# Kernel tuning notes

Hardware: AMD Instinct MI355X
Metric: run time of the kernel (lower is better)

The kernel has to match this reference:

```python
import jax, jax.numpy as jnp
import numpy as np

EPS = 1e-8
LN_EPS = 1e-5
PSCALE = 10.0
P = 8  # n_points


def _bb_frames(Xn, Xca, Xc):
    # Gram-Schmidt rigid frame from N, CA, C (AlphaFold rigids_from_3_points).
    v1 = Xc - Xca
    v2 = Xn - Xca
    e1 = v1 / jnp.sqrt(jnp.sum(v1 * v1, -1, keepdims=True) + EPS)
    u2 = v2 - e1 * jnp.sum(e1 * v2, -1, keepdims=True)
    e2 = u2 / jnp.sqrt(jnp.sum(u2 * u2, -1, keepdims=True) + EPS)
    e3 = jnp.cross(e1, e2)
    R = jnp.stack([e1, e2, e3], axis=-1)  # [B,N,3,3], columns are basis vectors
    t = Xca / PSCALE                      # scale_translation(1/position_scale)
    return R, t


def _layernorm(x, g, b):
    mu = jnp.mean(x, -1, keepdims=True)
    var = jnp.mean((x - mu) ** 2, -1, keepdims=True)
    return (x - mu) / jnp.sqrt(var + LN_EPS) * g + b


def setup_inputs() -> dict:
    key = jax.random.key(0)
    ks = jax.random.split(key, 24)
    B, N, K, D, H = 8, 512, 32, 128, 128
    msg_in = 2 * D + D + 9 * P  # 456
    s = 0.02
    inp = {
        "h_V": jax.random.normal(ks[0], (B, N, D), jnp.float32),
        "h_E": jax.random.normal(ks[1], (B, N, K, D), jnp.float32),
        "X": jax.random.normal(ks[2], (B, N, 3, 3), jnp.float32),
        "mask_V": jnp.ones((B, N), jnp.float32),
        "mask_attend": jnp.ones((B, N, K), jnp.float32),
        "Wp": jax.random.normal(ks[3], (D, P * 3), jnp.float32) * s,
        "bp": jnp.zeros((P * 3,), jnp.float32),
        "Wm1": jax.random.normal(ks[4], (msg_in, H), jnp.float32) * s,
        "bm1": jnp.zeros((H,), jnp.float32),
        "Wm2": jax.random.normal(ks[5], (H, H), jnp.float32) * s,
        "bm2": jnp.zeros((H,), jnp.float32),
        "Wm3": jax.random.normal(ks[6], (H, H), jnp.float32) * s,
        "bm3": jnp.zeros((H,), jnp.float32),
        "g1": jnp.ones((H,), jnp.float32),
        "be1": jnp.zeros((H,), jnp.float32),
        "Wd1": jax.random.normal(ks[7], (H, 4 * H), jnp.float32) * s,
        "bd1": jnp.zeros((4 * H,), jnp.float32),
        "Wd2": jax.random.normal(ks[8], (4 * H, H), jnp.float32) * s,
        "bd2": jnp.zeros((H,), jnp.float32),
        "g2": jnp.ones((H,), jnp.float32),
        "be2": jnp.zeros((H,), jnp.float32),
        "E_idx": jax.random.randint(ks[9], (B, N, K), 0, N, jnp.int32),
    }
    return inp


def reference(h_V, h_E, X, mask_V, mask_attend,
              Wp, bp, Wm1, bm1, Wm2, bm2, Wm3, bm3, g1, be1,
              Wd1, bd1, Wd2, bd2, g2, be2, E_idx):
    B, N, K = E_idx.shape
    R, t = _bb_frames(X[..., 0, :], X[..., 1, :], X[..., 2, :])
    # local points [B,N,P,3]
    p_local = (h_V @ Wp + bp).reshape(B, N, P, 3)
    # global points: R @ p + t
    p_global = jnp.einsum('bnij,bnpj->bnpi', R, p_local) + t[:, :, None, :]
    bidx = jnp.arange(B)[:, None, None]
    nbr_pg = p_global[bidx, E_idx]  # [B,N,K,P,3]
    nbr_hV = h_V[bidx, E_idx]       # [B,N,K,D]
    # distances in global frame
    diff = p_global[:, :, None] - nbr_pg
    npg_norm = jnp.sqrt(jnp.sum(diff * diff, -1) + EPS)  # [B,N,K,P]
    # neighbor points in local frame: R^T (q - t)
    q = nbr_pg - t[:, :, None, None, :]
    nbr_pl = jnp.einsum('bnij,bnkpi->bnkpj', R, q)       # [B,N,K,P,3]
    npl_norm = jnp.sqrt(jnp.sum(nbr_pl * nbr_pl, -1) + EPS)
    pl_norm = jnp.sqrt(jnp.sum(p_local * p_local, -1) + EPS)  # [B,N,P]

    D = h_V.shape[-1]
    node_expand = jnp.broadcast_to(h_V[:, :, None, :], (B, N, K, D))
    pl_flat = jnp.broadcast_to(p_local[:, :, None], (B, N, K, P, 3)).reshape(B, N, K, P * 3)
    pl_norm_e = jnp.broadcast_to(pl_norm[:, :, None, :], (B, N, K, P))
    msg_in = jnp.concatenate([
        node_expand, h_E, nbr_hV,
        pl_flat, pl_norm_e,
        nbr_pl.reshape(B, N, K, P * 3), npl_norm, npg_norm,
    ], axis=-1)

    # node_message_fn: 3-layer MLP with relu
    m = jax.nn.relu(msg_in @ Wm1 + bm1)
    m = jax.nn.relu(m @ Wm2 + bm2)
    m = m @ Wm3 + bm3
    m = m * mask_attend[..., None]
    node_m = jnp.mean(m, axis=-2)  # [B,N,H]

    h = _layernorm(h_V + node_m, g1, be1)  # dropout = identity (eval)
    dense = jax.nn.relu(h @ Wd1 + bd1) @ Wd2 + bd2
    h = _layernorm(h + dense, g2, be2)
    h = h * mask_V[..., None]
    return h, h_E
```

## Files before the change

kernel.cpp:

```cpp
#include <hip/hip_runtime.h>
#include <hip/hip_bf16.h>

typedef __hip_bfloat16 bf16;
typedef __attribute__((ext_vector_type(8))) short s16x8;
typedef __attribute__((ext_vector_type(4))) float f32x4;

#define DEV __device__ __forceinline__

DEV float us2f(unsigned short u){ return __uint_as_float(((unsigned int)u) << 16); }
DEV unsigned short f2us(float f){
    __hip_bfloat16 h = __float2bfloat16(f);
    unsigned short r; __builtin_memcpy(&r, &h, 2); return r;
}
DEV unsigned pack2(float a, float b){ return (unsigned)f2us(a) | ((unsigned)f2us(b) << 16); }

template<bool F32> DEV float ldf(const void* p, long i){
    if (F32) return reinterpret_cast<const float*>(p)[i];
    return us2f(reinterpret_cast<const unsigned short*>(p)[i]);
}
template<bool F32> DEV unsigned short ld16(const void* p, long i){
    if (F32) return f2us(reinterpret_cast<const float*>(p)[i]);
    return reinterpret_cast<const unsigned short*>(p)[i];
}

union U16x8 { uint4 u; s16x8 v; };

DEV bool is_f32(const void* maskV){
    return reinterpret_cast<const unsigned short*>(maskV)[0] != 0x3F80;
}

struct __align__(16) PreSmem {
    union __align__(16) {
        unsigned short lwT[128*40];
        struct {
            unsigned short lwp[24*132];
            float sX[2][9], sR[2][9], st3[2][3], spl[2][24], hvs[2][128];
        } pr;
    } u;
};

template<bool F32>
DEV void pre_prep(const void* hV, const void* X, const void* Wp, const void* bp,
                  float* pg, float* pl, float* pln, float* Rw, float* tw,
                  PreSmem& s, int bid, int tid)
{
    auto& pr = s.u.pr;
    for (int e = tid; e < 3072; e += 128) {
        int i = e / 24, j = e - i*24;
        pr.lwp[j*132 + i] = ld16<F32>(Wp, e);
    }
    const int wv = tid >> 6, ln = tid & 63;
    const int n = bid*2 + wv;
    if (ln < 9) pr.sX[wv][ln] = ldf<F32>(X, (long)n*9 + ln);
    for (int i = ln; i < 128; i += 64) pr.hvs[wv][i] = ldf<F32>(hV, (long)n*128 + i);
    __syncthreads();

    if (ln == 0) {
        float Nx=pr.sX[wv][0],Ny=pr.sX[wv][1],Nz=pr.sX[wv][2];
        float Ax=pr.sX[wv][3],Ay=pr.sX[wv][4],Az=pr.sX[wv][5];
        float Cx=pr.sX[wv][6],Cy=pr.sX[wv][7],Cz=pr.sX[wv][8];
        float v1x=Cx-Ax, v1y=Cy-Ay, v1z=Cz-Az;
        float v2x=Nx-Ax, v2y=Ny-Ay, v2z=Nz-Az;
        float r1 = 1.f/sqrtf(v1x*v1x+v1y*v1y+v1z*v1z + 1e-8f);
        float e1x=v1x*r1, e1y=v1y*r1, e1z=v1z*r1;
        float dp = e1x*v2x+e1y*v2y+e1z*v2z;
        float u2x=v2x-e1x*dp, u2y=v2y-e1y*dp, u2z=v2z-e1z*dp;
        float r2 = 1.f/sqrtf(u2x*u2x+u2y*u2y+u2z*u2z + 1e-8f);
        float e2x=u2x*r2, e2y=u2y*r2, e2z=u2z*r2;
        float e3x = e1y*e2z - e1z*e2y;
        float e3y = e1z*e2x - e1x*e2z;
        float e3z = e1x*e2y - e1y*e2x;
        pr.sR[wv][0]=e1x; pr.sR[wv][1]=e2x; pr.sR[wv][2]=e3x;
        pr.sR[wv][3]=e1y; pr.sR[wv][4]=e2y; pr.sR[wv][5]=e3y;
        pr.sR[wv][6]=e1z; pr.sR[wv][7]=e2z; pr.sR[wv][8]=e3z;
        pr.st3[wv][0]=Ax*0.1f; pr.st3[wv][1]=Ay*0.1f; pr.st3[wv][2]=Az*0.1f;
    }
    if (ln < 24) {
        float acc = ldf<F32>(bp, ln);
        const unsigned short* wr = &pr.lwp[ln*132];
        #pragma unroll
        for (int c=0;c<16;c++){
            #pragma unroll
            for (int k=0;k<8;k++)
                acc += pr.hvs[wv][c*8+k] * us2f(wr[c*8+k]);
        }
        pr.spl[wv][ln] = acc;
    }
    __syncthreads();

    if (ln < 24) {
        pl[n*24+ln] = pr.spl[wv][ln];
        int p = ln/3, c = ln - p*3;
        float g = pr.sR[wv][c*3+0]*pr.spl[wv][p*3+0] + pr.sR[wv][c*3+1]*pr.spl[wv][p*3+1]
                + pr.sR[wv][c*3+2]*pr.spl[wv][p*3+2] + pr.st3[wv][c];
        pg[n*24+ln] = g;
    }
    if (ln < 9) Rw[n*9+ln] = pr.sR[wv][ln];
    if (ln < 3) tw[n*3+ln] = pr.st3[wv][ln];
    if (ln < 8) {
        float a=pr.spl[wv][ln*3], b=pr.spl[wv][ln*3+1], c=pr.spl[wv][ln*3+2];
        pln[n*8+ln] = sqrtf(a*a+b*b+c*c + 1e-8f);
    }
}

template<bool F32>
DEV void pre_uv(const void* hV, const void* bm1, const void* Wm1,
                unsigned short* Uw, unsigned short* Vw,
                PreSmem& s, int r0, int tid)
{
    const int lane = tid & 63, w2 = tid >> 6;
    const int lm = lane & 15, quad = lane >> 4;

    s16x8 af[4];
    #pragma unroll
    for (int kc=0; kc<4; ++kc) {
        long src = (long)(r0 + lm)*128 + kc*32 + quad*8;
        U16x8 pk;
        if (F32) {
            const float4* vp = reinterpret_cast<const float4*>(reinterpret_cast<const float*>(hV) + src);
            float4 x = vp[0], y = vp[1];
            pk.u.x = pack2(x.x,x.y); pk.u.y = pack2(x.z,x.w);
            pk.u.z = pack2(y.x,y.y); pk.u.w = pack2(y.z,y.w);
        } else {
            pk.u = *reinterpret_cast<const uint4*>(reinterpret_cast<const unsigned short*>(hV) + src);
        }
        af[kc] = pk.v;
    }

    f32x4 accU[4], accV[4];
    #pragma unroll
    for (int nt=0; nt<4; ++nt) {
        float b0 = ldf<F32>(bm1, 64*w2 + nt*16 + lm);
        f32x4 iv = {b0,b0,b0,b0};
        accU[nt] = iv;
        f32x4 zv = {0.f,0.f,0.f,0.f};
        accV[nt] = zv;
    }

    for (int p=0; p<8; ++p) {
        int k0 = (p<4) ? p*32 : 256 + (p-4)*32;
        __syncthreads();
        for (int e = tid; e < 4096; e += 128) {
            int kk = e >> 7, c = e & 127;
            s.u.lwT[c*40 + kk] = ld16<F32>(Wm1, (long)k0*128 + e);
        }
        __syncthreads();
        s16x8 a = af[p & 3];
        #pragma unroll
        for (int nt=0; nt<4; ++nt) {
            s16x8 bf = *reinterpret_cast<const s16x8*>(&s.u.lwT[(64*w2 + nt*16 + lm)*40 + quad*8]);
            if (p < 4) accU[nt] = __builtin_amdgcn_mfma_f32_16x16x32_bf16(a, bf, accU[nt], 0,0,0);
            else       accV[nt] = __builtin_amdgcn_mfma_f32_16x16x32_bf16(a, bf, accV[nt], 0,0,0);
        }
    }
    #pragma unroll
    for (int nt=0; nt<4; ++nt)
        #pragma unroll
        for (int r=0; r<4; ++r) {
            long o = (long)(r0 + quad*4 + r)*128 + 64*w2 + nt*16 + lm;
            Uw[o] = f2us(accU[nt][r]);
            Vw[o] = f2us(accV[nt][r]);
        }
}

template<bool F32>
DEV void pre_wt(const void* Wm1, const void* Wm2, const void* Wm3,
                const void* Wd1, const void* Wd2,
                unsigned short* wt1, unsigned short* wt2, unsigned short* wt3,
                unsigned short* wd1T, unsigned short* wd2T, long t)
{
    if (t < 61440) {
        int k = (int)(t >> 7), h = (int)(t & 127);
        wt1[(long)h*480 + k] = (k < 456) ? ld16<F32>(Wm1, (long)k*128 + h) : (unsigned short)0;
    } else if (t < 77824) {
        long t2 = t - 61440; int k = (int)(t2 >> 7), h = (int)(t2 & 127);
        wt2[(long)h*128 + k] = ld16<F32>(Wm2, (long)k*128 + h);
    } else if (t < 94208) {
        long t2 = t - 77824; int k = (int)(t2 >> 7), h = (int)(t2 & 127);
        wt3[(long)h*128 + k] = ld16<F32>(Wm3, (long)k*128 + h);
    } else if (t < 159744) {
        long t2 = t - 94208; int k = (int)(t2 >> 9), n = (int)(t2 & 511);
        wd1T[(long)n*128 + k] = ld16<F32>(Wd1, (long)k*512 + n);
    } else {
        long t2 = t - 159744; int k = (int)(t2 >> 7), n = (int)(t2 & 127);
        wd2T[(long)n*512 + k] = ld16<F32>(Wd2, (long)k*128 + n);
    }
}

__global__ __launch_bounds__(128) void pre_k(
    const void* __restrict__ hV, const void* __restrict__ X,
    const void* __restrict__ Wp, const void* __restrict__ bp,
    const void* __restrict__ Wm1, const void* __restrict__ bm1,
    const void* __restrict__ Wm2, const void* __restrict__ Wm3,
    const void* __restrict__ Wd1, const void* __restrict__ Wd2,
    float* __restrict__ pg, float* __restrict__ pl, float* __restrict__ pln,
    float* __restrict__ Rw, float* __restrict__ tw,
    unsigned short* __restrict__ Uw, unsigned short* __restrict__ Vw,
    unsigned short* __restrict__ wt1, unsigned short* __restrict__ wt2,
    unsigned short* __restrict__ wt3, unsigned short* __restrict__ wd1T,
    unsigned short* __restrict__ wd2T, const void* __restrict__ maskV)
{
    __shared__ PreSmem s;
    int bid = blockIdx.x, tid = threadIdx.x;
    bool f32 = is_f32(maskV);
    if (bid < 2048) {
        if (f32) pre_prep<true >(hV,X,Wp,bp,pg,pl,pln,Rw,tw,s,bid,tid);
        else     pre_prep<false>(hV,X,Wp,bp,pg,pl,pln,Rw,tw,s,bid,tid);
    } else if (bid < 2304) {
        int r0 = (bid - 2048) * 16;
        if (f32) pre_uv<true >(hV,bm1,Wm1,Uw,Vw,s,r0,tid);
        else     pre_uv<false>(hV,bm1,Wm1,Uw,Vw,s,r0,tid);
    } else {
        long t = (long)(bid - 2304)*128 + tid;
        if (f32) pre_wt<true >(Wm1,Wm2,Wm3,Wd1,Wd2,wt1,wt2,wt3,wd1T,wd2T,t);
        else     pre_wt<false>(Wm1,Wm2,Wm3,Wd1,Wd2,wt1,wt2,wt3,wd1T,wd2T,t);
    }
}

#define ASTRIDE 40
#define MSTRIDE 136

struct __align__(16) Mp1Smem {
    union __align__(16) {
        unsigned short geo[3][64*ASTRIDE];
        unsigned short m[64*MSTRIDE];
    } u;
    int   sj[64];
    float smka[64];
    float spg[2][24], spl[2][24], spln[2][8], sR[2][9], st3[2][3];
    unsigned short sU[2*128];
};

template<bool F32>
DEV void mpnn1_body(
    const void* hV, const void* hE, const void* maskA,
    const void* bm2, const void* bm3, const int* Eidx,
    const float* pg, const float* pl, const float* pln,
    const float* Rw, const float* tw,
    const unsigned short* wt1, const unsigned short* wt2, const unsigned short* wt3,
    const unsigned short* Uw, const unsigned short* Vw,
    float* nodemsg, void* outE, Mp1Smem& sm, int n0, int tid)
{
    const int lane = tid & 63, w = tid >> 6;
    const int lm = lane & 15, quad = lane >> 4;

    if (tid < 64) { int l = tid >> 5;
        sm.sj[tid] = (((n0+l) >> 9) << 9) + Eidx[(long)(n0+l)*32 + (tid & 31)];
    } else { int t = tid - 64; int l = t >> 5;
        sm.smka[t] = ldf<F32>(maskA, (long)(n0+l)*32 + (t & 31));
    }
    if (tid < 48)        { sm.spg[tid/24][tid%24] = pg[(n0+tid/24)*24 + tid%24]; }
    else if (tid < 96)   { int t=tid-48; sm.spl[t/24][t%24] = pl[(n0+t/24)*24 + t%24]; }
    else if (tid < 112)  { int t=tid-96; sm.spln[t>>3][t&7]  = pln[(n0+(t>>3))*8 + (t&7)]; }
    if (tid < 18)        { sm.sR[tid/9][tid%9] = Rw[(n0+tid/9)*9 + tid%9]; }
    else if (tid < 24)   { int t=tid-18; sm.st3[t/3][t%3] = tw[(n0+t/3)*3 + t%3]; }
    for (int e = tid; e < 256; e += 128)
        sm.sU[e] = Uw[(long)(n0 + (e>>7))*128 + (e & 127)];
    __syncthreads();

    #pragma unroll
    for (int pass=0; pass<4; ++pass) {
        int v = tid + pass*128;
        int row = v >> 3, p = v & 7, nd = row >> 5;
        int j = sm.sj[row];
        float qx = pg[j*24 + p*3 + 0];
        float qy = pg[j*24 + p*3 + 1];
        float qz = pg[j*24 + p*3 + 2];
        float dx = sm.spg[nd][p*3+0]-qx, dy = sm.spg[nd][p*3+1]-qy, dz = sm.spg[nd][p*3+2]-qz;
        float npg = sqrtf(dx*dx+dy*dy+dz*dz + 1e-8f);
        float ux = qx - sm.st3[nd][0], uy = qy - sm.st3[nd][1], uz = qz - sm.st3[nd][2];
        float l0 = sm.sR[nd][0]*ux + sm.sR[nd][3]*uy + sm.sR[nd][6]*uz;
        float l1 = sm.sR[nd][1]*ux + sm.sR[nd][4]*uy + sm.sR[nd][7]*uz;
        float l2v= sm.sR[nd][2]*ux + sm.sR[nd][5]*uy + sm.sR[nd][8]*uz;
        float npl = sqrtf(l0*l0+l1*l1+l2v*l2v + 1e-8f);
        unsigned short* C0 = sm.u.geo[0];
        unsigned short* C1 = sm.u.geo[1];
        unsigned short* C2 = sm.u.geo[2];
        C0[row*ASTRIDE + p*3+0] = f2us(sm.spl[nd][p*3+0]);
        C0[row*ASTRIDE + p*3+1] = f2us(sm.spl[nd][p*3+1]);
        C0[row*ASTRIDE + p*3+2] = f2us(sm.spl[nd][p*3+2]);
        C0[row*ASTRIDE + 24+p]  = f2us(sm.spln[nd][p]);
        C1[row*ASTRIDE + p*3+0] = f2us(l0);
        C1[row*ASTRIDE + p*3+1] = f2us(l1);
        C1[row*ASTRIDE + p*3+2] = f2us(l2v);
        C1[row*ASTRIDE + 24+p]  = f2us(npl);
        C2[row*ASTRIDE + p]     = f2us(npg);
    }
    for (int z = tid; z < 64*24; z += 128) {
        int row = z / 24, col = 8 + (z % 24);
        sm.u.geo[2][row*ASTRIDE + col] = 0;
    }
    __syncthreads();

    const unsigned short* wr1[4];
    #pragma unroll
    for (int nt=0; nt<4; ++nt) wr1[nt] = wt1 + (long)(64*w + nt*16 + lm)*480 + quad*8;

    f32x4 acc[4][4];
    {
        f32x4 zv = {0.f,0.f,0.f,0.f};
        #pragma unroll
        for (int mt=0; mt<4; ++mt)
            #pragma unroll
            for (int nt=0; nt<4; ++nt) acc[mt][nt] = zv;
    }

    #pragma unroll
    for (int c=0; c<4; ++c) {
        s16x8 av[4];
        #pragma unroll
        for (int mt=0; mt<4; ++mt) {
            int row16 = 16*mt + lm, nd = mt >> 1;
            long src = ((long)(n0+nd)*32 + (row16&31))*128 + c*32 + quad*8;
            U16x8 pk;
            if (F32) {
                const float4* vp = reinterpret_cast<const float4*>(reinterpret_cast<const float*>(hE) + src);
                float4 x = vp[0], y = vp[1];
                if (w == 0) {
                    float4* d = reinterpret_cast<float4*>(reinterpret_cast<float*>(outE) + src);
                    d[0] = x; d[1] = y;
                }
                pk.u.x = pack2(x.x,x.y); pk.u.y = pack2(x.z,x.w);
                pk.u.z = pack2(y.x,y.y); pk.u.w = pack2(y.z,y.w);
            } else {
                pk.u = *reinterpret_cast<const uint4*>(reinterpret_cast<const unsigned short*>(hE) + src);
                if (w == 0)
                    *reinterpret_cast<uint4*>(reinterpret_cast<unsigned short*>(outE) + src) = pk.u;
            }
            av[mt] = pk.v;
        }
        #pragma unroll
        for (int nt=0; nt<4; ++nt) {
            s16x8 bf = *reinterpret_cast<const s16x8*>(wr1[nt] + (long)(c+4)*32);
            #pragma unroll
            for (int mt=0; mt<4; ++mt)
                acc[mt][nt] = __builtin_amdgcn_mfma_f32_16x16x32_bf16(av[mt], bf, acc[mt][nt], 0,0,0);
        }
    }
    #pragma unroll
    for (int c=0; c<3; ++c) {
        s16x8 av[4];
        #pragma unroll
        for (int mt=0; mt<4; ++mt)
            av[mt] = *reinterpret_cast<const s16x8*>(&sm.u.geo[c][(16*mt+lm)*ASTRIDE + quad*8]);
        #pragma unroll
        for (int nt=0; nt<4; ++nt) {
            s16x8 bf = *reinterpret_cast<const s16x8*>(wr1[nt] + (long)(c+12)*32);
            #pragma unroll
            for (int mt=0; mt<4; ++mt)
                acc[mt][nt] = __builtin_amdgcn_mfma_f32_16x16x32_bf16(av[mt], bf, acc[mt][nt], 0,0,0);
        }
    }
    __syncthreads();

    #pragma unroll
    for (int mt=0; mt<4; ++mt)
        #pragma unroll
        for (int nt=0; nt<4; ++nt)
            #pragma unroll
            for (int r=0; r<4; ++r)
                sm.u.m[(16*mt + quad*4 + r)*MSTRIDE + 64*w + nt*16 + lm]
                    = f2us(acc[mt][nt][r]);

    const int row = tid >> 1, ch = tid & 1;
    const int jv = sm.sj[row];
    const unsigned short* vrow = Vw + (long)jv*128 + ch*64;
    uint4 pv[8];
    #pragma unroll
    for (int b=0;b<8;++b) pv[b] = *reinterpret_cast<const uint4*>(vrow + b*8);
    __syncthreads();

    {
        unsigned short* mrow = &sm.u.m[row*MSTRIDE + ch*64];
        const unsigned short* urow = &sm.sU[(row>>5)*128 + ch*64];
        #pragma unroll
        for (int b=0;b<8;++b) {
            U16x8 vm; vm.u = *reinterpret_cast<const uint4*>(mrow + b*8);
            U16x8 vv; vv.u = pv[b];
            float f[8];
            #pragma unroll
            for (int i=0;i<8;++i)
                f[i] = fmaxf(us2f((unsigned short)vm.v[i]) + us2f((unsigned short)vv.v[i])
                             + us2f(urow[b*8+i]), 0.f);
            uint4 o;
            o.x = pack2(f[0],f[1]); o.y = pack2(f[2],f[3]);
            o.z = pack2(f[4],f[5]); o.w = pack2(f[6],f[7]);
            *reinterpret_cast<uint4*>(mrow + b*8) = o;
        }
    }
    __syncthreads();

    #pragma unroll
    for (int nt=0; nt<4; ++nt) {
        float b0 = ldf<F32>(bm2, 64*w + nt*16 + lm);
        f32x4 iv = {b0,b0,b0,b0};
        #pragma unroll
        for (int mt=0; mt<4; ++mt) acc[mt][nt] = iv;
    }
    #pragma unroll
    for (int kc=0; kc<4; ++kc) {
        s16x8 av[4];
        #pragma unroll
        for (int mt=0; mt<4; ++mt)
            av[mt] = *reinterpret_cast<const s16x8*>(&sm.u.m[(16*mt+lm)*MSTRIDE + kc*32 + quad*8]);
        #pragma unroll
        for (int nt=0; nt<4; ++nt) {
            s16x8 bf = *reinterpret_cast<const s16x8*>(&wt2[(long)(64*w + nt*16 + lm)*128 + kc*32 + quad*8]);
            #pragma unroll
            for (int mt=0; mt<4; ++mt)
                acc[mt][nt] = __builtin_amdgcn_mfma_f32_16x16x32_bf16(av[mt], bf, acc[mt][nt], 0,0,0);
        }
    }
    __syncthreads();

    #pragma unroll
    for (int mt=0; mt<4; ++mt)
        #pragma unroll
        for (int nt=0; nt<4; ++nt)
            #pragma unroll
            for (int r=0; r<4; ++r)
                sm.u.m[(16*mt + quad*4 + r)*MSTRIDE + 64*w + nt*16 + lm]
                    = f2us(fmaxf(acc[mt][nt][r], 0.f));
    __syncthreads();

    #pragma unroll
    for (int nt=0; nt<4; ++nt) {
        float b0 = ldf<F32>(bm3, 64*w + nt*16 + lm);
        f32x4 iv = {b0,b0,b0,b0};
        #pragma unroll
        for (int mt=0; mt<4; ++mt) acc[mt][nt] = iv;
    }
    #pragma unroll
    for (int kc=0; kc<4; ++kc) {
        s16x8 av[4];
        #pragma unroll
        for (int mt=0; mt<4; ++mt)
            av[mt] = *reinterpret_cast<const s16x8*>(&sm.u.m[(16*mt+lm)*MSTRIDE + kc*32 + quad*8]);
        #pragma unroll
        for (int nt=0; nt<4; ++nt) {
            s16x8 bf = *reinterpret_cast<const s16x8*>(&wt3[(long)(64*w + nt*16 + lm)*128 + kc*32 + quad*8]);
            #pragma unroll
            for (int mt=0; mt<4; ++mt)
                acc[mt][nt] = __builtin_amdgcn_mfma_f32_16x16x32_bf16(av[mt], bf, acc[mt][nt], 0,0,0);
        }
    }

    #pragma unroll
    for (int nt=0; nt<4; ++nt) {
        float s0 = 0.f, s1 = 0.f;
        #pragma unroll
        for (int r=0; r<4; ++r) {
            s0 += acc[0][nt][r] * sm.smka[     quad*4 + r]
                + acc[1][nt][r] * sm.smka[16 + quad*4 + r];
            s1 += acc[2][nt][r] * sm.smka[32 + quad*4 + r]
                + acc[3][nt][r] * sm.smka[48 + quad*4 + r];
        }
        s0 += __shfl_xor(s0, 16); s0 += __shfl_xor(s0, 32);
        s1 += __shfl_xor(s1, 16); s1 += __shfl_xor(s1, 32);
        if (lane < 16) {
            nodemsg[(long)(n0  )*128 + 64*w + nt*16 + lane] = s0;
            nodemsg[(long)(n0+1)*128 + 64*w + nt*16 + lane] = s1;
        }
    }
}

__global__ __launch_bounds__(128) void mpnn1_k(
    const void* __restrict__ hV, const void* __restrict__ hE,
    const void* __restrict__ maskV, const void* __restrict__ maskA,
    const void* __restrict__ bm2, const void* __restrict__ bm3,
    const int* __restrict__ Eidx,
    const float* __restrict__ pg, const float* __restrict__ pl,
    const float* __restrict__ pln, const float* __restrict__ Rw,
    const float* __restrict__ tw,
    const unsigned short* __restrict__ wt1, const unsigned short* __restrict__ wt2,
    const unsigned short* __restrict__ wt3,
    const unsigned short* __restrict__ Uw, const unsigned short* __restrict__ Vw,
    float* __restrict__ nodemsg, void* __restrict__ dout)
{
    __shared__ Mp1Smem sm;
    int n0 = blockIdx.x * 2, tid = threadIdx.x;
    if (is_f32(maskV)) {
        void* outE = reinterpret_cast<float*>(dout) + 524288;
        mpnn1_body<true >(hV,hE,maskA,bm2,bm3,Eidx,pg,pl,pln,Rw,tw,wt1,wt2,wt3,Uw,Vw,nodemsg,outE,sm,n0,tid);
    } else {
        void* outE = reinterpret_cast<unsigned short*>(dout) + 524288;
        mpnn1_body<false>(hV,hE,maskA,bm2,bm3,Eidx,pg,pl,pln,Rw,tw,wt1,wt2,wt3,Uw,Vw,nodemsg,outE,sm,n0,tid);
    }
}

#define TSTRIDE 520

struct __align__(16) FfnSmem {
    unsigned short x1[16*MSTRIDE];
    union __align__(16) {
        unsigned short t1[16*TSTRIDE];
        float yf[16*132];
    } u;
};

template<bool F32>
DEV void ffn_body(const void* hV, const void* maskV, const float* nodemsg,
                  const void* g1, const void* be1, const void* bd1, const void* bd2,
                  const void* g2, const void* be2,
                  const unsigned short* wd1T, const unsigned short* wd2T,
                  void* out, FfnSmem& sm, int n0, int tid)
{
    const int lane = tid & 63, w = tid >> 6;
    const int lm = lane & 15, quad = lane >> 4;

    {
        const int r = tid >> 4, c0 = (tid & 15) * 8;
        const long nb = (long)(n0 + r)*128;
        float xv[8];
        float s1 = 0.f, s2 = 0.f;
        #pragma unroll
        for (int j=0; j<8; ++j) {
            float v = ldf<F32>(hV, nb + c0 + j) + nodemsg[nb + c0 + j] * (1.f/32.f);
            xv[j] = v; s1 += v; s2 += v*v;
        }
        s1 += __shfl_xor(s1,1); s1 += __shfl_xor(s1,2);
        s1 += __shfl_xor(s1,4); s1 += __shfl_xor(s1,8);
        s2 += __shfl_xor(s2,1); s2 += __shfl_xor(s2,2);
        s2 += __shfl_xor(s2,4); s2 += __shfl_xor(s2,8);
        float mu = s1 * (1.f/128.f);
        float var = s2 * (1.f/128.f) - mu*mu;
        float rs = 1.f/sqrtf(var + 1e-5f);
        #pragma unroll
        for (int j=0; j<8; ++j) {
            int c = c0 + j;
            sm.x1[r*MSTRIDE + c] = f2us((xv[j]-mu)*rs*ldf<F32>(g1, c) + ldf<F32>(be1, c));
        }
    }
    __syncthreads();

    {
        f32x4 t1a[8];
        #pragma unroll
        for (int nt=0; nt<8; ++nt) {
            float b0 = ldf<F32>(bd1, 128*w + nt*16 + lm);
            f32x4 iv = {b0,b0,b0,b0};
            t1a[nt] = iv;
        }
        #pragma unroll
        for (int kc=0; kc<4; ++kc) {
            s16x8 a = *reinterpret_cast<const s16x8*>(&sm.x1[lm*MSTRIDE + kc*32 + quad*8]);
            #pragma unroll
            for (int nt=0; nt<8; ++nt) {
                s16x8 bf = *reinterpret_cast<const s16x8*>(&wd1T[(long)(128*w + nt*16 + lm)*128 + kc*32 + quad*8]);
                t1a[nt] = __builtin_amdgcn_mfma_f32_16x16x32_bf16(a, bf, t1a[nt], 0,0,0);
            }
        }
        #pragma unroll
        for (int nt=0; nt<8; ++nt)
            #pragma unroll
            for (int r=0; r<4; ++r)
                sm.u.t1[(quad*4 + r)*TSTRIDE + 128*w + nt*16 + lm] = f2us(fmaxf(t1a[nt][r], 0.f));
    }
    __syncthreads();

    f32x4 yacc[2];
    #pragma unroll
    for (int nt=0; nt<2; ++nt) {
        float b0 = ldf<F32>(bd2, 32*w + nt*16 + lm);
        f32x4 iv = {b0,b0,b0,b0};
        yacc[nt] = iv;
    }
    #pragma unroll
    for (int kc=0; kc<16; ++kc) {
        s16x8 a = *reinterpret_cast<const s16x8*>(&sm.u.t1[lm*TSTRIDE + kc*32 + quad*8]);
        #pragma unroll
        for (int nt=0; nt<2; ++nt) {
            s16x8 bf = *reinterpret_cast<const s16x8*>(&wd2T[(long)(32*w + nt*16 + lm)*512 + kc*32 + quad*8]);
            yacc[nt] = __builtin_amdgcn_mfma_f32_16x16x32_bf16(a, bf, yacc[nt], 0,0,0);
        }
    }
    __syncthreads();

    #pragma unroll
    for (int nt=0; nt<2; ++nt)
        #pragma unroll
        for (int r=0; r<4; ++r) {
            int rr = quad*4 + r, c = 32*w + nt*16 + lm;
            sm.u.yf[rr*132 + c] = yacc[nt][r] + us2f(sm.x1[rr*MSTRIDE + c]);
        }
    __syncthreads();

    {
        const int r = tid >> 4, c0 = (tid & 15) * 8;
        float yv[8];
        float s1 = 0.f, s2 = 0.f;
        #pragma unroll
        for (int j=0; j<8; ++j) {
            float v = sm.u.yf[r*132 + c0 + j];
            yv[j] = v; s1 += v; s2 += v*v;
        }
        s1 += __shfl_xor(s1,1); s1 += __shfl_xor(s1,2);
        s1 += __shfl_xor(s1,4); s1 += __shfl_xor(s1,8);
        s2 += __shfl_xor(s2,1); s2 += __shfl_xor(s2,2);
        s2 += __shfl_xor(s2,4); s2 += __shfl_xor(s2,8);
        float mu = s1 * (1.f/128.f);
        float var = s2 * (1.f/128.f) - mu*mu;
        float rs = 1.f/sqrtf(var + 1e-5f);
        float mv = ldf<F32>(maskV, n0 + r);
        const long ob = (long)(n0 + r)*128 + c0;
        #pragma unroll
        for (int j=0; j<8; ++j) {
            int c = c0 + j;
            float v = ((yv[j]-mu)*rs*ldf<F32>(g2, c) + ldf<F32>(be2, c)) * mv;
            if (F32) reinterpret_cast<float*>(out)[ob + j] = v;
            else     reinterpret_cast<unsigned short*>(out)[ob + j] = f2us(v);
        }
    }
}

__global__ __launch_bounds__(256) void ffn_k(
    const void* __restrict__ hV, const void* __restrict__ maskV,
    const float* __restrict__ nodemsg,
    const void* __restrict__ g1, const void* __restrict__ be1,
    const void* __restrict__ bd1, const void* __restrict__ bd2,
    const void* __restrict__ g2, const void* __restrict__ be2,
    const unsigned short* __restrict__ wd1T, const unsigned short* __restrict__ wd2T,
    void* __restrict__ out)
{
    __shared__ FfnSmem sm;
    int n0 = blockIdx.x * 16, tid = threadIdx.x;
    if (is_f32(maskV))
        ffn_body<true >(hV,maskV,nodemsg,g1,be1,bd1,bd2,g2,be2,wd1T,wd2T,out,sm,n0,tid);
    else
        ffn_body<false>(hV,maskV,nodemsg,g1,be1,bd1,bd2,g2,be2,wd1T,wd2T,out,sm,n0,tid);
}

extern "C" void kernel_launch(void* const* d_in, const int* in_sizes, int n_in,
                              void* d_out, int out_size, void* d_ws, size_t ws_size,
                              hipStream_t stream)
{
    const void* hV    = d_in[0];
    const void* hE    = d_in[1];
    const void* X     = d_in[2];
    const void* maskV = d_in[3];
    const void* maskA = d_in[4];
    const void* Wp    = d_in[5];
    const void* bp    = d_in[6];
    const void* Wm1   = d_in[7];
    const void* bm1   = d_in[8];
    const void* Wm2   = d_in[9];
    const void* bm2   = d_in[10];
    const void* Wm3   = d_in[11];
    const void* bm3   = d_in[12];
    const void* g1    = d_in[13];
    const void* be1   = d_in[14];
    const void* Wd1   = d_in[15];
    const void* bd1   = d_in[16];
    const void* Wd2   = d_in[17];
    const void* bd2   = d_in[18];
    const void* g2    = d_in[19];
    const void* be2   = d_in[20];
    const int*  Eidx  = (const int*)d_in[21];

    float* ws = (float*)d_ws;
    float* pg  = ws;
    float* pl  = ws + 98304;
    float* pln = ws + 196608;
    float* Rw  = ws + 229376;
    float* tw  = ws + 266240;
    float* nm  = ws + 278528;
    unsigned short* wt1  = (unsigned short*)(ws + 802816);
    unsigned short* wt2  = wt1 + 61440;
    unsigned short* wt3  = wt2 + 16384;
    unsigned short* wd1T = wt3 + 16384;
    unsigned short* wd2T = wd1T + 65536;
    unsigned short* Uw   = wd2T + 65536;
    unsigned short* Vw   = Uw + 524288;

    pre_k<<<4064, 128, 0, stream>>>(hV, X, Wp, bp, Wm1, bm1, Wm2, Wm3, Wd1, Wd2,
                                    pg, pl, pln, Rw, tw, Uw, Vw,
                                    wt1, wt2, wt3, wd1T, wd2T, maskV);

    mpnn1_k<<<2048, 128, 0, stream>>>(hV, hE, maskV, maskA, bm2, bm3, Eidx,
                                      pg, pl, pln, Rw, tw, wt1, wt2, wt3,
                                      Uw, Vw, nm, d_out);

    ffn_k<<<256, 256, 0, stream>>>(hV, maskV, nm, g1, be1, bd1, bd2, g2, be2,
                                   wd1T, wd2T, d_out);
}
```

Measured before the change: 245.0 us.

## Prefetch gathers, double-buffer hE chunks, raise mpnn occupancy, widen FFN blocks

In the message kernel, the neighbor point gathers are issued together before any geometry math, and hE chunks are double-buffered in registers so the next chunk's global loads overlap the current chunk's MFMAs. launch_bounds gains a minimum of 4 blocks per CU to push occupancy. The FFN kernel moves from 256 to 512 threads per block, giving each wave fewer output tiles and adjusting the layernorm reductions to match. Together these aim to hide memory latency and add parallelism, at the cost of more register pressure and a possible spill risk from the occupancy hint.

```diff
diff --git a/kernel.cpp b/kernel.cpp
--- a/kernel.cpp
+++ b/kernel.cpp
@@ -233,7 +233,7 @@
 
 template<bool F32>
 DEV void mpnn1_body(
-    const void* hV, const void* hE, const void* maskA,
+    const void* hE, const void* maskA,
     const void* bm2, const void* bm3, const int* Eidx,
     const float* pg, const float* pl, const float* pln,
     const float* Rw, const float* tw,
@@ -258,33 +258,42 @@
         sm.sU[e] = Uw[(long)(n0 + (e>>7))*128 + (e & 127)];
     __syncthreads();
 
-    #pragma unroll
-    for (int pass=0; pass<4; ++pass) {
-        int v = tid + pass*128;
-        int row = v >> 3, p = v & 7, nd = row >> 5;
-        int j = sm.sj[row];
-        float qx = pg[j*24 + p*3 + 0];
-        float qy = pg[j*24 + p*3 + 1];
-        float qz = pg[j*24 + p*3 + 2];
-        float dx = sm.spg[nd][p*3+0]-qx, dy = sm.spg[nd][p*3+1]-qy, dz = sm.spg[nd][p*3+2]-qz;
-        float npg = sqrtf(dx*dx+dy*dy+dz*dz + 1e-8f);
-        float ux = qx - sm.st3[nd][0], uy = qy - sm.st3[nd][1], uz = qz - sm.st3[nd][2];
-        float l0 = sm.sR[nd][0]*ux + sm.sR[nd][3]*uy + sm.sR[nd][6]*uz;
-        float l1 = sm.sR[nd][1]*ux + sm.sR[nd][4]*uy + sm.sR[nd][7]*uz;
-        float l2v= sm.sR[nd][2]*ux + sm.sR[nd][5]*uy + sm.sR[nd][8]*uz;
-        float npl = sqrtf(l0*l0+l1*l1+l2v*l2v + 1e-8f);
-        unsigned short* C0 = sm.u.geo[0];
-        unsigned short* C1 = sm.u.geo[1];
-        unsigned short* C2 = sm.u.geo[2];
-        C0[row*ASTRIDE + p*3+0] = f2us(sm.spl[nd][p*3+0]);
-        C0[row*ASTRIDE + p*3+1] = f2us(sm.spl[nd][p*3+1]);
-        C0[row*ASTRIDE + p*3+2] = f2us(sm.spl[nd][p*3+2]);
-        C0[row*ASTRIDE + 24+p]  = f2us(sm.spln[nd][p]);
-        C1[row*ASTRIDE + p*3+0] = f2us(l0);
-        C1[row*ASTRIDE + p*3+1] = f2us(l1);
-        C1[row*ASTRIDE + p*3+2] = f2us(l2v);
-        C1[row*ASTRIDE + 24+p]  = f2us(npl);
-        C2[row*ASTRIDE + p]     = f2us(npg);
+    {
+        float q_[4][3];
+        #pragma unroll
+        for (int pass=0; pass<4; ++pass) {
+            int v = tid + pass*128;
+            int row = v >> 3, p = v & 7;
+            int j = sm.sj[row];
+            q_[pass][0] = pg[j*24 + p*3 + 0];
+            q_[pass][1] = pg[j*24 + p*3 + 1];
+            q_[pass][2] = pg[j*24 + p*3 + 2];
+        }
+        #pragma unroll
+        for (int pass=0; pass<4; ++pass) {
+            int v = tid + pass*128;
+            int row = v >> 3, p = v & 7, nd = row >> 5;
+            float qx = q_[pass][0], qy = q_[pass][1], qz = q_[pass][2];
+            float dx = sm.spg[nd][p*3+0]-qx, dy = sm.spg[nd][p*3+1]-qy, dz = sm.spg[nd][p*3+2]-qz;
+            float npg = sqrtf(dx*dx+dy*dy+dz*dz + 1e-8f);
+            float ux = qx - sm.st3[nd][0], uy = qy - sm.st3[nd][1], uz = qz - sm.st3[nd][2];
+            float l0 = sm.sR[nd][0]*ux + sm.sR[nd][3]*uy + sm.sR[nd][6]*uz;
+            float l1 = sm.sR[nd][1]*ux + sm.sR[nd][4]*uy + sm.sR[nd][7]*uz;
+            float l2v= sm.sR[nd][2]*ux + sm.sR[nd][5]*uy + sm.sR[nd][8]*uz;
+            float npl = sqrtf(l0*l0+l1*l1+l2v*l2v + 1e-8f);
+            unsigned short* C0 = sm.u.geo[0];
+            unsigned short* C1 = sm.u.geo[1];
+            unsigned short* C2 = sm.u.geo[2];
+            C0[row*ASTRIDE + p*3+0] = f2us(sm.spl[nd][p*3+0]);
+            C0[row*ASTRIDE + p*3+1] = f2us(sm.spl[nd][p*3+1]);
+            C0[row*ASTRIDE + p*3+2] = f2us(sm.spl[nd][p*3+2]);
+            C0[row*ASTRIDE + 24+p]  = f2us(sm.spln[nd][p]);
+            C1[row*ASTRIDE + p*3+0] = f2us(l0);
+            C1[row*ASTRIDE + p*3+1] = f2us(l1);
+            C1[row*ASTRIDE + p*3+2] = f2us(l2v);
+            C1[row*ASTRIDE + 24+p]  = f2us(npl);
+            C2[row*ASTRIDE + p]     = f2us(npg);
+        }
     }
     for (int z = tid; z < 64*24; z += 128) {
         int row = z / 24, col = 8 + (z % 24);
@@ -305,14 +314,11 @@
             for (int nt=0; nt<4; ++nt) acc[mt][nt] = zv;
     }
 
-    #pragma unroll
-    for (int c=0; c<4; ++c) {
-        s16x8 av[4];
+    auto loadChunk = [&](int c, U16x8* dst) {
         #pragma unroll
         for (int mt=0; mt<4; ++mt) {
             int row16 = 16*mt + lm, nd = mt >> 1;
-            long src = ((long)(n0+nd)*32 + (row16&31))*128 + c*32 + quad*8;
-            U16x8 pk;
+            long src = ((long)(n0+nd)*32 + (row16&31))*128 + (long)c*32 + quad*8;
             if (F32) {
                 const float4* vp = reinterpret_cast<const float4*>(reinterpret_cast<const float*>(hE) + src);
                 float4 x = vp[0], y = vp[1];
@@ -320,21 +326,30 @@
                     float4* d = reinterpret_cast<float4*>(reinterpret_cast<float*>(outE) + src);
                     d[0] = x; d[1] = y;
                 }
-                pk.u.x = pack2(x.x,x.y); pk.u.y = pack2(x.z,x.w);
-                pk.u.z = pack2(y.x,y.y); pk.u.w = pack2(y.z,y.w);
+                dst[mt].u.x = pack2(x.x,x.y); dst[mt].u.y = pack2(x.z,x.w);
+                dst[mt].u.z = pack2(y.x,y.y); dst[mt].u.w = pack2(y.z,y.w);
             } else {
-                pk.u = *reinterpret_cast<const uint4*>(reinterpret_cast<const unsigned short*>(hE) + src);
+                dst[mt].u = *reinterpret_cast<const uint4*>(reinterpret_cast<const unsigned short*>(hE) + src);
                 if (w == 0)
-                    *reinterpret_cast<uint4*>(reinterpret_cast<unsigned short*>(outE) + src) = pk.u;
+                    *reinterpret_cast<uint4*>(reinterpret_cast<unsigned short*>(outE) + src) = dst[mt].u;
             }
-            av[mt] = pk.v;
-        }
-        #pragma unroll
-        for (int nt=0; nt<4; ++nt) {
-            s16x8 bf = *reinterpret_cast<const s16x8*>(wr1[nt] + (long)(c+4)*32);
-            #pragma unroll
-            for (int mt=0; mt<4; ++mt)
-                acc[mt][nt] = __builtin_amdgcn_mfma_f32_16x16x32_bf16(av[mt], bf, acc[mt][nt], 0,0,0);
+        }
+    };
+
+    {
+        U16x8 pkA[4], pkB[4];
+        loadChunk(0, pkA);
+        #pragma unroll
+        for (int c=0; c<4; ++c) {
+            U16x8* cur = (c & 1) ? pkB : pkA;
+            if (c < 3) loadChunk(c+1, (c & 1) ? pkA : pkB);
+            #pragma unroll
+            for (int nt=0; nt<4; ++nt) {
+                s16x8 bf = *reinterpret_cast<const s16x8*>(wr1[nt] + (long)(c+4)*32);
+                #pragma unroll
+                for (int mt=0; mt<4; ++mt)
+                    acc[mt][nt] = __builtin_amdgcn_mfma_f32_16x16x32_bf16(cur[mt].v, bf, acc[mt][nt], 0,0,0);
+            }
         }
     }
     #pragma unroll
@@ -464,8 +479,8 @@
     }
 }
 
-__global__ __launch_bounds__(128) void mpnn1_k(
-    const void* __restrict__ hV, const void* __restrict__ hE,
+__global__ __launch_bounds__(128, 4) void mpnn1_k(
+    const void* __restrict__ hE,
     const void* __restrict__ maskV, const void* __restrict__ maskA,
     const void* __restrict__ bm2, const void* __restrict__ bm3,
     const int* __restrict__ Eidx,
@@ -481,10 +496,10 @@
     int n0 = blockIdx.x * 2, tid = threadIdx.x;
     if (is_f32(maskV)) {
         void* outE = reinterpret_cast<float*>(dout) + 524288;
-        mpnn1_body<true >(hV,hE,maskA,bm2,bm3,Eidx,pg,pl,pln,Rw,tw,wt1,wt2,wt3,Uw,Vw,nodemsg,outE,sm,n0,tid);
+        mpnn1_body<true >(hE,maskA,bm2,bm3,Eidx,pg,pl,pln,Rw,tw,wt1,wt2,wt3,Uw,Vw,nodemsg,outE,sm,n0,tid);
     } else {
         void* outE = reinterpret_cast<unsigned short*>(dout) + 524288;
-        mpnn1_body<false>(hV,hE,maskA,bm2,bm3,Eidx,pg,pl,pln,Rw,tw,wt1,wt2,wt3,Uw,Vw,nodemsg,outE,sm,n0,tid);
+        mpnn1_body<false>(hE,maskA,bm2,bm3,Eidx,pg,pl,pln,Rw,tw,wt1,wt2,wt3,Uw,Vw,nodemsg,outE,sm,n0,tid);
     }
 }
 
@@ -509,24 +524,24 @@
     const int lm = lane & 15, quad = lane >> 4;
 
     {
-        const int r = tid >> 4, c0 = (tid & 15) * 8;
+        const int r = tid >> 5, c0 = (tid & 31) * 4;
         const long nb = (long)(n0 + r)*128;
-        float xv[8];
+        float xv[4];
         float s1 = 0.f, s2 = 0.f;
         #pragma unroll
-        for (int j=0; j<8; ++j) {
+        for (int j=0; j<4; ++j) {
             float v = ldf<F32>(hV, nb + c0 + j) + nodemsg[nb + c0 + j] * (1.f/32.f);
             xv[j] = v; s1 += v; s2 += v*v;
         }
-        s1 += __shfl_xor(s1,1); s1 += __shfl_xor(s1,2);
-        s1 += __shfl_xor(s1,4); s1 += __shfl_xor(s1,8);
-        s2 += __shfl_xor(s2,1); s2 += __shfl_xor(s2,2);
-        s2 += __shfl_xor(s2,4); s2 += __shfl_xor(s2,8);
+        s1 += __shfl_xor(s1,1); s1 += __shfl_xor(s1,2); s1 += __shfl_xor(s1,4);
+        s1 += __shfl_xor(s1,8); s1 += __shfl_xor(s1,16);
+        s2 += __shfl_xor(s2,1); s2 += __shfl_xor(s2,2); s2 += __shfl_xor(s2,4);
+        s2 += __shfl_xor(s2,8); s2 += __shfl_xor(s2,16);
         float mu = s1 * (1.f/128.f);
         float var = s2 * (1.f/128.f) - mu*mu;
         float rs = 1.f/sqrtf(var + 1e-5f);
         #pragma unroll
-        for (int j=0; j<8; ++j) {
+        for (int j=0; j<4; ++j) {
             int c = c0 + j;
             sm.x1[r*MSTRIDE + c] = f2us((xv[j]-mu)*rs*ldf<F32>(g1, c) + ldf<F32>(be1, c));
         }
@@ -534,10 +549,10 @@
     __syncthreads();
 
     {
-        f32x4 t1a[8];
-        #pragma unroll
-        for (int nt=0; nt<8; ++nt) {
-            float b0 = ldf<F32>(bd1, 128*w + nt*16 + lm);
+        f32x4 t1a[4];
+        #pragma unroll
+        for (int nt=0; nt<4; ++nt) {
+            float b0 = ldf<F32>(bd1, 64*w + nt*16 + lm);
             f32x4 iv = {b0,b0,b0,b0};
             t1a[nt] = iv;
         }
@@ -545,66 +560,60 @@
         for (int kc=0; kc<4; ++kc) {
             s16x8 a = *reinterpret_cast<const s16x8*>(&sm.x1[lm*MSTRIDE + kc*32 + quad*8]);
             #pragma unroll
-            for (int nt=0; nt<8; ++nt) {
-                s16x8 bf = *reinterpret_cast<const s16x8*>(&wd1T[(long)(128*w + nt*16 + lm)*128 + kc*32 + quad*8]);
+            for (int nt=0; nt<4; ++nt) {
+                s16x8 bf = *reinterpret_cast<const s16x8*>(&wd1T[(long)(64*w + nt*16 + lm)*128 + kc*32 + quad*8]);
                 t1a[nt] = __builtin_amdgcn_mfma_f32_16x16x32_bf16(a, bf, t1a[nt], 0,0,0);
             }
         }
         #pragma unroll
-        for (int nt=0; nt<8; ++nt)
+        for (int nt=0; nt<4; ++nt)
             #pragma unroll
             for (int r=0; r<4; ++r)
-                sm.u.t1[(quad*4 + r)*TSTRIDE + 128*w + nt*16 + lm] = f2us(fmaxf(t1a[nt][r], 0.f));
-    }
-    __syncthreads();
-
-    f32x4 yacc[2];
-    #pragma unroll
-    for (int nt=0; nt<2; ++nt) {
-        float b0 = ldf<F32>(bd2, 32*w + nt*16 + lm);
+                sm.u.t1[(quad*4 + r)*TSTRIDE + 64*w + nt*16 + lm] = f2us(fmaxf(t1a[nt][r], 0.f));
+    }
+    __syncthreads();
+
+    f32x4 yacc;
+    {
+        float b0 = ldf<F32>(bd2, 16*w + lm);
         f32x4 iv = {b0,b0,b0,b0};
-        yacc[nt] = iv;
+        yacc = iv;
     }
     #pragma unroll
     for (int kc=0; kc<16; ++kc) {
         s16x8 a = *reinterpret_cast<const s16x8*>(&sm.u.t1[lm*TSTRIDE + kc*32 + quad*8]);
-        #pragma unroll
-        for (int nt=0; nt<2; ++nt) {
-            s16x8 bf = *reinterpret_cast<const s16x8*>(&wd2T[(long)(32*w + nt*16 + lm)*512 + kc*32 + quad*8]);
-            yacc[nt] = __builtin_amdgcn_mfma_f32_16x16x32_bf16(a, bf, yacc[nt], 0,0,0);
-        }
-    }
-    __syncthreads();
-
-    #pragma unroll
-    for (int nt=0; nt<2; ++nt)
-        #pragma unroll
-        for (int r=0; r<4; ++r) {
-            int rr = quad*4 + r, c = 32*w + nt*16 + lm;
-            sm.u.yf[rr*132 + c] = yacc[nt][r] + us2f(sm.x1[rr*MSTRIDE + c]);
-        }
-    __syncthreads();
-
-    {
-        const int r = tid >> 4, c0 = (tid & 15) * 8;
-        float yv[8];
+        s16x8 bf = *reinterpret_cast<const s16x8*>(&wd2T[(long)(16*w + lm)*512 + kc*32 + quad*8]);
+        yacc = __builtin_amdgcn_mfma_f32_16x16x32_bf16(a, bf, yacc, 0,0,0);
+    }
+    __syncthreads();
+
+    #pragma unroll
+    for (int r=0; r<4; ++r) {
+        int rr = quad*4 + r, c = 16*w + lm;
+        sm.u.yf[rr*132 + c] = yacc[r] + us2f(sm.x1[rr*MSTRIDE + c]);
+    }
+    __syncthreads();
+
+    {
+        const int r = tid >> 5, c0 = (tid & 31) * 4;
+        float yv[4];
         float s1 = 0.f, s2 = 0.f;
         #pragma unroll
-        for (int j=0; j<8; ++j) {
+        for (int j=0; j<4; ++j) {
             float v = sm.u.yf[r*132 + c0 + j];
             yv[j] = v; s1 += v; s2 += v*v;
         }
-        s1 += __shfl_xor(s1,1); s1 += __shfl_xor(s1,2);
-        s1 += __shfl_xor(s1,4); s1 += __shfl_xor(s1,8);
-        s2 += __shfl_xor(s2,1); s2 += __shfl_xor(s2,2);
-        s2 += __shfl_xor(s2,4); s2 += __shfl_xor(s2,8);
+        s1 += __shfl_xor(s1,1); s1 += __shfl_xor(s1,2); s1 += __shfl_xor(s1,4);
+        s1 += __shfl_xor(s1,8); s1 += __shfl_xor(s1,16);
+        s2 += __shfl_xor(s2,1); s2 += __shfl_xor(s2,2); s2 += __shfl_xor(s2,4);
+        s2 += __shfl_xor(s2,8); s2 += __shfl_xor(s2,16);
         float mu = s1 * (1.f/128.f);
         float var = s2 * (1.f/128.f) - mu*mu;
         float rs = 1.f/sqrtf(var + 1e-5f);
         float mv = ldf<F32>(maskV, n0 + r);
         const long ob = (long)(n0 + r)*128 + c0;
         #pragma unroll
-        for (int j=0; j<8; ++j) {
+        for (int j=0; j<4; ++j) {
             int c = c0 + j;
             float v = ((yv[j]-mu)*rs*ldf<F32>(g2, c) + ldf<F32>(be2, c)) * mv;
             if (F32) reinterpret_cast<float*>(out)[ob + j] = v;
@@ -613,7 +622,7 @@
     }
 }
 
-__global__ __launch_bounds__(256) void ffn_k(
+__global__ __launch_bounds__(512) void ffn_k(
     const void* __restrict__ hV, const void* __restrict__ maskV,
     const float* __restrict__ nodemsg,
     const void* __restrict__ g1, const void* __restrict__ be1,
@@ -676,10 +685,10 @@
                                     pg, pl, pln, Rw, tw, Uw, Vw,
                                     wt1, wt2, wt3, wd1T, wd2T, maskV);
 
-    mpnn1_k<<<2048, 128, 0, stream>>>(hV, hE, maskV, maskA, bm2, bm3, Eidx,
+    mpnn1_k<<<2048, 128, 0, stream>>>(hE, maskV, maskA, bm2, bm3, Eidx,
                                       pg, pl, pln, Rw, tw, wt1, wt2, wt3,
                                       Uw, Vw, nm, d_out);
 
-    ffn_k<<<256, 256, 0, stream>>>(hV, maskV, nm, g1, be1, bd1, bd2, g2, be2,
+    ffn_k<<<256, 512, 0, stream>>>(hV, maskV, nm, g1, be1, bd1, bd2, g2, be2,
                                    wd1T, wd2T, d_out);
 }
```

Result: slower. 275.5 us (+12.5%).
